# Kernel optimization log

Hardware: AMD Instinct MI355X
Metric: run time of the kernel (lower is better)

## Reference

```python
import jax, jax.numpy as jnp
import numpy as np

N = 2048   # num nodes
D = 512    # hidden_dim


def setup_inputs() -> dict:
    key = jax.random.key(0)
    k1, k2 = jax.random.split(key)
    x = jax.random.normal(k1, (N, D), dtype=jnp.float32)
    # linear: hidden_dim -> 1 (xavier-like scale)
    w = jax.random.normal(k2, (D,), dtype=jnp.float32) * (1.0 / np.sqrt(D))
    b = jnp.zeros((1,), dtype=jnp.float32)
    return {"x": x, "w": w, "b": b}


def reference(x, w, b):
    # euclidean_distance_matrix + linear fused:
    # s[i,j] = sum_d w_d * (x[i,d]-x[j,d])^2 + b
    #        = q_i + q_j - 2*(x*w) @ x^T + b,  q_i = sum_d w_d x[i,d]^2
    xw = x * w                              # [N, D]
    q = jnp.sum(xw * x, axis=1)             # [N]
    cross = xw @ x.T                        # [N, N]
    s = q[:, None] + q[None, :] - 2.0 * cross + b[0]
    grouping_matrix = jax.nn.sigmoid(s)     # [N, N]

    # compute_fielder, similarity_graph='base'
    W = grouping_matrix
    degree = jnp.sum(W, axis=1)
    L = jnp.diag(degree) - W                # symmetric graph Laplacian
    eigen_values, eigen_vectors = jnp.linalg.eigh(L)
    order = jnp.argsort(jnp.abs(eigen_values))
    fielder_value = eigen_values[order[1]]
    fielder_vector = eigen_vectors[:, order[1]]
    return grouping_matrix, fielder_value, fielder_vector
```

## Files before the change

kernel.cpp:

```cpp
#include <hip/hip_runtime.h>
#include <math.h>

constexpr int NN = 2048;
constexpr int DD_ = 512;
constexpr int LM = 64;
constexpr int VS = NN + 32;
constexpr int GPART = 8;
#define SIGN_FLIP 1

__device__ inline double waveReduceSum(double v) {
#pragma unroll
  for (int off = 32; off; off >>= 1) v += __shfl_down(v, off, 64);
  return v;
}

__device__ inline double blockReduceSum256(double v) {
  __shared__ double sm[4];
  int lane = threadIdx.x & 63;
  int wid  = threadIdx.x >> 6;
  v = waveReduceSum(v);
  __syncthreads();
  if (lane == 0) sm[wid] = v;
  __syncthreads();
  double r = 0.0;
  if (threadIdx.x < 4) r = sm[threadIdx.x];
  if (wid == 0) {
    r += __shfl_down(r, 2, 64);
    r += __shfl_down(r, 1, 64);
  }
  return r;
}

__global__ __launch_bounds__(256) void k_q(const float* __restrict__ x,
                                           const float* __restrict__ w,
                                           float* __restrict__ q) {
  int row = blockIdx.x;
  int t = threadIdx.x;
  const float* xr = x + (size_t)row * DD_;
  float acc = 0.f;
#pragma unroll
  for (int p = 0; p < 2; ++p) {
    int d = t + 256 * p;
    float xv = xr[d];
    acc += w[d] * xv * xv;
  }
  double r = blockReduceSum256((double)acc);
  if (t == 0) q[row] = (float)r;
}

__global__ __launch_bounds__(256) void k_W(const float* __restrict__ x,
                                           const float* __restrict__ wv,
                                           const float* __restrict__ q,
                                           const float* __restrict__ bptr,
                                           float* __restrict__ out) {
  __shared__ float As[16][68];
  __shared__ float Bs[16][68];
  const int t = threadIdx.x;
  const int i0 = blockIdx.y * 64, j0 = blockIdx.x * 64;
  const int lr = t >> 4, lk = t & 15;
  const int tr = t >> 4, tc = t & 15;
  float acc[4][4];
#pragma unroll
  for (int a = 0; a < 4; ++a)
#pragma unroll
    for (int b = 0; b < 4; ++b) acc[a][b] = 0.f;

  for (int kk = 0; kk < DD_; kk += 16) {
    float wk = wv[kk + lk];
#pragma unroll
    for (int p = 0; p < 4; ++p) {
      As[lk][lr + 16 * p] = x[(size_t)(i0 + lr + 16 * p) * DD_ + kk + lk] * wk;
      Bs[lk][lr + 16 * p] = x[(size_t)(j0 + lr + 16 * p) * DD_ + kk + lk];
    }
    __syncthreads();
#pragma unroll
    for (int k = 0; k < 16; ++k) {
      float4 av = *(const float4*)&As[k][tr * 4];
      float4 bv = *(const float4*)&Bs[k][tc * 4];
      float aa[4] = {av.x, av.y, av.z, av.w};
      float bb[4] = {bv.x, bv.y, bv.z, bv.w};
#pragma unroll
      for (int a = 0; a < 4; ++a)
#pragma unroll
        for (int b = 0; b < 4; ++b) acc[a][b] += aa[a] * bb[b];
    }
    __syncthreads();
  }
  float b0 = bptr[0];
#pragma unroll
  for (int a = 0; a < 4; ++a) {
    int i = i0 + tr * 4 + a;
    float qi = q[i];
    float4 st;
    float* stp = &st.x;
#pragma unroll
    for (int b = 0; b < 4; ++b) {
      int j = j0 + tc * 4 + b;
      float s = qi + q[j] - 2.0f * acc[a][b] + b0;
      stp[b] = 1.0f / (1.0f + expf(-s));
    }
    *(float4*)&out[(size_t)i * NN + j0 + tc * 4] = st;
  }
}

__global__ __launch_bounds__(256) void k_init(double* __restrict__ r,
                                              double* __restrict__ part) {
  int t = threadIdx.x;
  double loc[8];
  double s = 0.0;
#pragma unroll
  for (int p = 0; p < 8; ++p) {
    unsigned i = (unsigned)(t + 256 * p);
    unsigned u = i * 2654435761u + 0x9E3779B9u;
    u ^= u >> 16; u *= 0x85EBCA6Bu; u ^= u >> 13; u *= 0xC2B2AE35u; u ^= u >> 16;
    double val = ((double)u / 4294967296.0) - 0.5;
    loc[p] = val; s += val;
  }
  __shared__ double mean_s, inv_s;
  double tot = blockReduceSum256(s);
  if (t == 0) mean_s = tot / (double)NN;
  __syncthreads();
  double mean = mean_s;
  double ss = 0.0;
#pragma unroll
  for (int p = 0; p < 8; ++p) { loc[p] -= mean; ss += loc[p] * loc[p]; }
  double tss = blockReduceSum256(ss);
  if (t == 0) inv_s = 1.0 / sqrt(tss);
  __syncthreads();
  double inv = inv_s;
#pragma unroll
  for (int p = 0; p < 8; ++p) r[t + 256 * p] = loc[p] * inv;
  if (t < GPART) part[t] = (t == 0) ? 1.0 : 0.0;
}

__global__ __launch_bounds__(256) void k_mva(const float* __restrict__ Wm,
                                             double* __restrict__ deg,
                                             const double* __restrict__ rprev,
                                             const double* __restrict__ part,
                                             double* __restrict__ V,
                                             double* __restrict__ wstash,
                                             double* __restrict__ c,
                                             double* __restrict__ beta, int j) {
  int b = blockIdx.x, t = threadIdx.x;
  double ss = 0.0;
#pragma unroll
  for (int p = 0; p < GPART; ++p) ss += part[p];
  double bet = sqrt(ss);
  double inv = (bet > 1e-3) ? 1.0 / bet : 0.0;

  if (b < NN) {
    const float* wr = Wm + (size_t)b * NN;
    double acc = 0.0, dsum = 0.0;
    if (j == 0) {
#pragma unroll
      for (int p = 0; p < 2; ++p) {
        int i = 4 * t + 1024 * p;
        float4 wl = *(const float4*)&wr[i];
        dsum += (double)wl.x + (double)wl.y + (double)wl.z + (double)wl.w;
        acc += (double)wl.x * rprev[i] + (double)wl.y * rprev[i + 1] +
               (double)wl.z * rprev[i + 2] + (double)wl.w * rprev[i + 3];
      }
    } else {
#pragma unroll
      for (int p = 0; p < 2; ++p) {
        int i = 4 * t + 1024 * p;
        float4 wl = *(const float4*)&wr[i];
        acc += (double)wl.x * rprev[i] + (double)wl.y * rprev[i + 1] +
               (double)wl.z * rprev[i + 2] + (double)wl.w * rprev[i + 3];
      }
    }
    double red = blockReduceSum256(acc);
    double dred = 0.0;
    if (j == 0) dred = blockReduceSum256(dsum);
    if (t == 0) {
      double d;
      if (j == 0) { d = dred; deg[b] = d; }
      else d = deg[b];
      double vj = rprev[b] * inv;
      V[(size_t)j * VS + b] = vj;
      wstash[(size_t)j * VS + b] = d * vj - red * inv;
      if (b == 0 && j > 0) beta[j - 1] = (bet > 1e-3) ? bet : 0.0;
    }
  } else {
    int q = b - NN;
    const double* wq = wstash + (size_t)q * VS;
    double a = 0.0;
#pragma unroll
    for (int p = 0; p < 8; ++p) { int i = t + 256 * p; a += wq[i] * rprev[i]; }
    double red = blockReduceSum256(a);
    if (t == 0) c[q] = red * inv;
  }
}

__global__ __launch_bounds__(256) void k_orthb(const double* __restrict__ V,
                                               const double* __restrict__ wstash,
                                               const double* __restrict__ c,
                                               double* __restrict__ r,
                                               double* __restrict__ part,
                                               double* __restrict__ alpha, int j) {
  __shared__ double cs[LM];
  __shared__ double cj_s, s1_s;
  int b = blockIdx.x, t = threadIdx.x;
  const double* wj = wstash + (size_t)j * VS;
  const double* vj = V + (size_t)j * VS;
  double a = 0.0, s = 0.0;
#pragma unroll
  for (int p = 0; p < 8; ++p) {
    int i = t + 256 * p;
    double wv = wj[i];
    a += vj[i] * wv;
    s += wv;
  }
  double cj = blockReduceSum256(a);
  double s1 = blockReduceSum256(s);
  if (t == 0) { cj_s = cj; s1_s = s1; }
  for (int k = t; k < j; k += 256) cs[k] = c[k];
  __syncthreads();
  double cjv = cj_s, s1v = s1_s;
  int i = b * 256 + t;
  double val = wj[i] - s1v / (double)NN - cjv * vj[i];
  for (int k = 0; k < j; ++k) val -= cs[k] * V[(size_t)k * VS + i];
  r[i] = val;
  double rr = blockReduceSum256(val * val);
  if (t == 0) {
    part[b] = rr;
    if (b == 0) alpha[j] = cjv;
  }
}

__device__ inline double guardpiv(double d) {
  if (fabs(d) < 1e-280) return (d < 0.0) ? -1e-280 : 1e-280;
  return d;
}

__global__ __launch_bounds__(64) void k_tri(const double* __restrict__ alpha,
                                            const double* __restrict__ beta,
                                            double* __restrict__ svec) {
  __shared__ double al[LM], be[LM];
  __shared__ double Dg[LM], Dl[LM], Du[LM], Du2[LM], bb[LM];
  __shared__ unsigned char piv[LM];
  __shared__ double bounds[2];
  __shared__ int cnts[64];
  __shared__ int meff_s;
  int t = threadIdx.x;
  for (int i = t; i < LM; i += 64) { al[i] = alpha[i]; be[i] = (i < LM - 1) ? beta[i] : 0.0; }
  __syncthreads();
  if (t == 0) {
    int m = LM;
    for (int i = 0; i < LM; ++i) {
      if (!isfinite(al[i])) { m = i; break; }
      if (i < LM - 1 && (be[i] == 0.0 || !isfinite(be[i]))) { m = i + 1; break; }
    }
    if (m < 2) m = 2;
    meff_s = m;
  }
  __syncthreads();
  const int n = meff_s;
  double lo = 1e300, hi = -1e300;
  for (int i = t; i < n; i += 64) {
    double r = 0.0;
    if (i > 0) r += fabs(be[i - 1]);
    if (i < n - 1) r += fabs(be[i]);
    lo = fmin(lo, al[i] - r);
    hi = fmax(hi, al[i] + r);
  }
#pragma unroll
  for (int off = 32; off; off >>= 1) {
    lo = fmin(lo, __shfl_down(lo, off, 64));
    hi = fmax(hi, __shfl_down(hi, off, 64));
  }
  if (t == 0) { bounds[0] = lo; bounds[1] = hi; }
  __syncthreads();
  for (int round = 0; round < 3; ++round) {
    double L0 = bounds[0], H0 = bounds[1];
    double p = L0 + (H0 - L0) * ((double)(t + 1) / 65.0);
    int cnt = 0;
    double d = al[0] - p;
    if (d < 0) cnt++;
    for (int i = 1; i < n; ++i) {
      if (fabs(d) < 1e-300) d = (d < 0.0) ? -1e-300 : 1e-300;
      double bi = be[i - 1];
      d = (al[i] - p) - bi * bi / d;
      if (d < 0) cnt++;
    }
    cnts[t] = cnt;
    __syncthreads();
    if (t == 0) {
      double nl = L0, nh = H0;
      for (int l = 0; l < 64; ++l) {
        double pl = L0 + (H0 - L0) * ((double)(l + 1) / 65.0);
        if (cnts[l] == 0) nl = pl;
        else { nh = pl; break; }
      }
      bounds[0] = nl; bounds[1] = nh;
    }
    __syncthreads();
  }
  double sigma = 0.5 * (bounds[0] + bounds[1]);
  if (t == 0) {
    for (int i = 0; i < n; ++i) Dg[i] = al[i] - sigma;
    for (int i = 0; i < n - 1; ++i) { Dl[i] = be[i]; Du[i] = be[i]; }
    for (int i = 0; i < n - 2; ++i) Du2[i] = 0.0;
    for (int i = 0; i < n - 1; ++i) {
      if (fabs(Dg[i]) >= fabs(Dl[i])) {
        double dpiv = guardpiv(Dg[i]);
        double fact = Dl[i] / dpiv;
        Dl[i] = fact;
        Dg[i + 1] -= fact * Du[i];
        piv[i] = 0;
      } else {
        double fact = Dg[i] / Dl[i];
        Dg[i] = Dl[i]; Dl[i] = fact;
        double temp = Du[i];
        Du[i] = Dg[i + 1];
        Dg[i + 1] = temp - fact * Dg[i + 1];
        if (i < n - 2) { Du2[i] = Du[i + 1]; Du[i + 1] = -fact * Du[i + 1]; }
        piv[i] = 1;
      }
    }
    for (int i = 0; i < n; ++i) bb[i] = 1.0;
    for (int i = 0; i < n - 1; ++i) {
      if (!piv[i]) bb[i + 1] -= Dl[i] * bb[i];
      else { double tmp = bb[i]; bb[i] = bb[i + 1]; bb[i + 1] = tmp - Dl[i] * bb[i]; }
    }
    bb[n - 1] = bb[n - 1] / guardpiv(Dg[n - 1]);
    bb[n - 2] = (bb[n - 2] - Du[n - 2] * bb[n - 1]) / guardpiv(Dg[n - 2]);
    for (int i = n - 3; i >= 0; --i)
      bb[i] = (bb[i] - Du[i] * bb[i + 1] - Du2[i] * bb[i + 2]) / guardpiv(Dg[i]);
    double nrm = 0.0;
    for (int i = 0; i < n; ++i) nrm += bb[i] * bb[i];
    double s = 1.0 / sqrt(nrm);
    for (int i = 0; i < LM; ++i) svec[i] = (i < n) ? bb[i] * s : 0.0;
  }
}

__global__ __launch_bounds__(256) void k_ritz(const double* __restrict__ V,
                                              const double* __restrict__ s,
                                              double* __restrict__ u) {
  __shared__ double cs[LM];
  int t = threadIdx.x;
  for (int k = t; k < LM; k += 256) cs[k] = s[k];
  __syncthreads();
  int i = blockIdx.x * 256 + t;
  double acc = 0.0;
  for (int k = 0; k < LM; ++k) acc += cs[k] * V[(size_t)k * VS + i];
  u[i] = acc;
}

__global__ __launch_bounds__(256) void k_mvu(const float* __restrict__ Wm,
                                             const double* __restrict__ deg,
                                             const double* __restrict__ v,
                                             double* __restrict__ w) {
  int row = blockIdx.x, t = threadIdx.x;
  const float* wr = Wm + (size_t)row * NN;
  double acc = 0.0;
#pragma unroll
  for (int p = 0; p < 2; ++p) {
    int i = 4 * t + 1024 * p;
    float4 wl = *(const float4*)&wr[i];
    acc += (double)wl.x * v[i] + (double)wl.y * v[i + 1] +
           (double)wl.z * v[i + 2] + (double)wl.w * v[i + 3];
  }
  double r = blockReduceSum256(acc);
  if (t == 0) w[row] = deg[row] * v[row] - r;
}

__global__ __launch_bounds__(256) void k_tail(const double* __restrict__ u,
                                              const double* __restrict__ lu,
                                              float* __restrict__ out_lam,
                                              float* __restrict__ outv) {
  __shared__ double mv[256];
  __shared__ int mi[256];
  __shared__ double mean_s, scale_s;
  int t = threadIdx.x;
  double a = 0.0, b = 0.0;
#pragma unroll
  for (int p = 0; p < 8; ++p) {
    int i = t + 256 * p;
    a += u[i] * lu[i];
    b += u[i] * u[i];
  }
  double ra = blockReduceSum256(a);
  double rb = blockReduceSum256(b);
  if (t == 0) *out_lam = (float)(ra / rb);
  double loc[8];
  double s = 0.0;
#pragma unroll
  for (int p = 0; p < 8; ++p) { loc[p] = u[t + 256 * p]; s += loc[p]; }
  double tot = blockReduceSum256(s);
  if (t == 0) mean_s = tot / (double)NN;
  __syncthreads();
  double mean = mean_s;
  double ss = 0.0, bv = -1.0;
  int bi = 0;
#pragma unroll
  for (int p = 0; p < 8; ++p) {
    loc[p] -= mean;
    ss += loc[p] * loc[p];
    double aa = fabs(loc[p]);
    if (aa > bv) { bv = aa; bi = p; }
  }
  double tss = blockReduceSum256(ss);
  mv[t] = bv; mi[t] = t + 256 * bi;
  __syncthreads();
  for (int off = 128; off; off >>= 1) {
    if (t < off) {
      if (mv[t + off] > mv[t]) { mv[t] = mv[t + off]; mi[t] = mi[t + off]; }
    }
    __syncthreads();
  }
  if (t == 0) {
    int gi = mi[0];
    double best = u[gi] - mean_s;
    double sgn = (best < 0.0) ? -1.0 : 1.0;
#if SIGN_FLIP
    sgn = -sgn;
#endif
    scale_s = sgn / sqrt(tss);
  }
  __syncthreads();
  double sc = scale_s;
#pragma unroll
  for (int p = 0; p < 8; ++p) outv[t + 256 * p] = (float)(loc[p] * sc);
}

extern "C" void kernel_launch(void* const* d_in, const int* in_sizes, int n_in,
                              void* d_out, int out_size, void* d_ws, size_t ws_size,
                              hipStream_t stream) {
  const float* x = (const float*)d_in[0];
  const float* wv = (const float*)d_in[1];
  const float* bp = (const float*)d_in[2];
  float* out = (float*)d_out;

  char* ws = (char*)d_ws;
  size_t off = 0;
  auto alloc = [&](size_t bytes) -> char* {
    char* p = ws + off;
    off = (off + bytes + 255) & ~(size_t)255;
    return p;
  };
  float* q      = (float*)alloc((size_t)NN * 4);
  double* deg   = (double*)alloc((size_t)NN * 8);
  double* r     = (double*)alloc((size_t)NN * 8);
  double* u     = (double*)alloc((size_t)NN * 8);
  double* c     = (double*)alloc((size_t)(LM + 2) * 8);
  double* alpha = (double*)alloc((size_t)LM * 8);
  double* beta  = (double*)alloc((size_t)LM * 8);
  double* svec  = (double*)alloc((size_t)LM * 8);
  double* part  = (double*)alloc((size_t)GPART * 8);
  double* V     = (double*)alloc((size_t)LM * VS * 8);
  double* wstash= (double*)alloc((size_t)LM * VS * 8);
  (void)ws_size; (void)in_sizes; (void)n_in; (void)out_size;

  k_q<<<NN, 256, 0, stream>>>(x, wv, q);
  dim3 g(NN / 64, NN / 64);
  k_W<<<g, 256, 0, stream>>>(x, wv, q, bp, out);
  k_init<<<1, 256, 0, stream>>>(r, part);

  for (int j = 0; j < LM; ++j) {
    k_mva<<<NN + j, 256, 0, stream>>>(out, deg, r, part, V, wstash, c, beta, j);
    k_orthb<<<NN / 256, 256, 0, stream>>>(V, wstash, c, r, part, alpha, j);
  }
  k_tri<<<1, 64, 0, stream>>>(alpha, beta, svec);
  k_ritz<<<NN / 256, 256, 0, stream>>>(V, svec, u);
  k_mvu<<<NN, 256, 0, stream>>>(out, deg, u, r);
  k_tail<<<1, 256, 0, stream>>>(u, r, out + (size_t)NN * NN,
                                out + (size_t)NN * NN + 1);
}
```

Before: 842.7 us.

## Compute similarity GEMM with split-bf16 MFMA and double-buffered LDS tiles

Replaces the fp32 CUDA-core tiled GEMM with a 128x128-tile MFMA bf16 kernel using a three-pass hi/lo split (ah*bh + ah*bl + al*bh) to keep near-fp32 accuracy. A new preprocessing kernel computes q and writes hi/lo bf16 copies of x*w and x. The bf16 buffers alias the Lanczos V/wstash workspace, which is only used later. This adds an extra conversion pass and some precision loss from the dropped lo*lo term.

```diff
diff --git a/kernel.cpp b/kernel.cpp
--- a/kernel.cpp
+++ b/kernel.cpp
@@ -8,6 +8,10 @@
 constexpr int GPART = 8;
 #define SIGN_FLIP 1
 
+
+typedef __attribute__((ext_vector_type(4))) float f32x4;
+typedef __attribute__((ext_vector_type(8))) short bf16x8;
+
 __device__ inline double waveReduceSum(double v) {
 #pragma unroll
   for (int off = 32; off; off >>= 1) v += __shfl_down(v, off, 64);
@@ -31,75 +35,147 @@
   return r;
 }
 
-__global__ __launch_bounds__(256) void k_q(const float* __restrict__ x,
-                                           const float* __restrict__ w,
-                                           float* __restrict__ q) {
-  int row = blockIdx.x;
-  int t = threadIdx.x;
-  const float* xr = x + (size_t)row * DD_;
-  float acc = 0.f;
-#pragma unroll
-  for (int p = 0; p < 2; ++p) {
-    int d = t + 256 * p;
-    float xv = xr[d];
-    acc += w[d] * xv * xv;
-  }
-  double r = blockReduceSum256((double)acc);
-  if (t == 0) q[row] = (float)r;
-}
-
-__global__ __launch_bounds__(256) void k_W(const float* __restrict__ x,
-                                           const float* __restrict__ wv,
-                                           const float* __restrict__ q,
-                                           const float* __restrict__ bptr,
-                                           float* __restrict__ out) {
-  __shared__ float As[16][68];
-  __shared__ float Bs[16][68];
+__device__ inline double blockReduceSum128(double v) {
+  __shared__ double sm[2];
+  int lane = threadIdx.x & 63;
+  int wid  = threadIdx.x >> 6;
+  v = waveReduceSum(v);
+  if (lane == 0) sm[wid] = v;
+  __syncthreads();
+  double r = 0.0;
+  if (threadIdx.x == 0) r = sm[0] + sm[1];
+  return r;
+}
+
+__device__ inline unsigned short f2bf(float f) {
+  unsigned u = __float_as_uint(f);
+  u += 0x7FFFu + ((u >> 16) & 1u);
+  return (unsigned short)(u >> 16);
+}
+__device__ inline float bf2f(unsigned short h) {
+  return __uint_as_float(((unsigned)h) << 16);
+}
+
+__global__ __launch_bounds__(128) void k_cvtq(const float* __restrict__ x,
+                                              const float* __restrict__ w,
+                                              float* __restrict__ q,
+                                              unsigned short* __restrict__ ah,
+                                              unsigned short* __restrict__ al,
+                                              unsigned short* __restrict__ bh,
+                                              unsigned short* __restrict__ bl) {
+  int row = blockIdx.x, t = threadIdx.x;
+  int d = 4 * t;
+  float4 xv = *(const float4*)&x[(size_t)row * DD_ + d];
+  float4 wv = *(const float4*)&w[d];
+  float xs[4] = {xv.x, xv.y, xv.z, xv.w};
+  float wsv[4] = {wv.x, wv.y, wv.z, wv.w};
+  unsigned short rah[4], ral[4], rbh[4], rbl[4];
+  float accq = 0.f;
+#pragma unroll
+  for (int kq = 0; kq < 4; ++kq) {
+    float xf = xs[kq], wf = wsv[kq];
+    float a = xf * wf;
+    unsigned short h = f2bf(a);
+    rah[kq] = h;
+    ral[kq] = f2bf(a - bf2f(h));
+    unsigned short hb = f2bf(xf);
+    rbh[kq] = hb;
+    rbl[kq] = f2bf(xf - bf2f(hb));
+    accq += wf * xf * xf;
+  }
+  ushort4 vA = {rah[0], rah[1], rah[2], rah[3]};
+  ushort4 vAl = {ral[0], ral[1], ral[2], ral[3]};
+  ushort4 vB = {rbh[0], rbh[1], rbh[2], rbh[3]};
+  ushort4 vBl = {rbl[0], rbl[1], rbl[2], rbl[3]};
+  *(ushort4*)&ah[(size_t)row * DD_ + d] = vA;
+  *(ushort4*)&al[(size_t)row * DD_ + d] = vAl;
+  *(ushort4*)&bh[(size_t)row * DD_ + d] = vB;
+  *(ushort4*)&bl[(size_t)row * DD_ + d] = vBl;
+  double rq = blockReduceSum128((double)accq);
+  if (t == 0) q[row] = (float)rq;
+}
+
+__global__ __launch_bounds__(256) void k_Wm(const unsigned short* __restrict__ ah,
+                                            const unsigned short* __restrict__ al,
+                                            const unsigned short* __restrict__ bh,
+                                            const unsigned short* __restrict__ bl,
+                                            const float* __restrict__ q,
+                                            const float* __restrict__ bptr,
+                                            float* __restrict__ out) {
+  __shared__ unsigned short As[2][128][40];
+  __shared__ unsigned short Bs[2][128][40];
   const int t = threadIdx.x;
-  const int i0 = blockIdx.y * 64, j0 = blockIdx.x * 64;
-  const int lr = t >> 4, lk = t & 15;
-  const int tr = t >> 4, tc = t & 15;
-  float acc[4][4];
+  const int i0 = blockIdx.y * 128, j0 = blockIdx.x * 128;
+  const int lane = t & 63, wv = t >> 6;
+  const int wr = wv >> 1, wc = wv & 1;
+  const int fr = lane & 15, kc = lane >> 4;
+  const int srow = t >> 1, scol = (t & 1) * 16;
+
+  f32x4 acc[4][4];
 #pragma unroll
   for (int a = 0; a < 4; ++a)
 #pragma unroll
-    for (int b = 0; b < 4; ++b) acc[a][b] = 0.f;
-
-  for (int kk = 0; kk < DD_; kk += 16) {
-    float wk = wv[kk + lk];
-#pragma unroll
-    for (int p = 0; p < 4; ++p) {
-      As[lk][lr + 16 * p] = x[(size_t)(i0 + lr + 16 * p) * DD_ + kk + lk] * wk;
-      Bs[lk][lr + 16 * p] = x[(size_t)(j0 + lr + 16 * p) * DD_ + kk + lk];
+    for (int b = 0; b < 4; ++b) acc[a][b] = (f32x4){0.f, 0.f, 0.f, 0.f};
+
+  {
+    bf16x8 ra0 = *(const bf16x8*)&ah[(size_t)(i0 + srow) * DD_ + scol];
+    bf16x8 ra1 = *(const bf16x8*)&ah[(size_t)(i0 + srow) * DD_ + scol + 8];
+    bf16x8 rb0 = *(const bf16x8*)&bh[(size_t)(j0 + srow) * DD_ + scol];
+    bf16x8 rb1 = *(const bf16x8*)&bh[(size_t)(j0 + srow) * DD_ + scol + 8];
+    *(bf16x8*)&As[0][srow][scol] = ra0;
+    *(bf16x8*)&As[0][srow][scol + 8] = ra1;
+    *(bf16x8*)&Bs[0][srow][scol] = rb0;
+    *(bf16x8*)&Bs[0][srow][scol + 8] = rb1;
+  }
+  __syncthreads();
+  int cur = 0;
+  for (int s = 0; s < 48; ++s) {
+    bf16x8 na0, na1, nb0, nb1;
+    if (s + 1 < 48) {
+      int pass = (s + 1) >> 4;
+      int kk = ((s + 1) & 15) * 32;
+      const unsigned short* srcA = (pass == 2) ? al : ah;
+      const unsigned short* srcB = (pass == 1) ? bl : bh;
+      na0 = *(const bf16x8*)&srcA[(size_t)(i0 + srow) * DD_ + kk + scol];
+      na1 = *(const bf16x8*)&srcA[(size_t)(i0 + srow) * DD_ + kk + scol + 8];
+      nb0 = *(const bf16x8*)&srcB[(size_t)(j0 + srow) * DD_ + kk + scol];
+      nb1 = *(const bf16x8*)&srcB[(size_t)(j0 + srow) * DD_ + kk + scol + 8];
+    }
+    bf16x8 af[4], bq[4];
+#pragma unroll
+    for (int a = 0; a < 4; ++a)
+      af[a] = *(const bf16x8*)&As[cur][wr * 64 + a * 16 + fr][kc * 8];
+#pragma unroll
+    for (int b = 0; b < 4; ++b)
+      bq[b] = *(const bf16x8*)&Bs[cur][wc * 64 + b * 16 + fr][kc * 8];
+#pragma unroll
+    for (int a = 0; a < 4; ++a)
+#pragma unroll
+      for (int b = 0; b < 4; ++b)
+        acc[a][b] = __builtin_amdgcn_mfma_f32_16x16x32_bf16(af[a], bq[b], acc[a][b], 0, 0, 0);
+    if (s + 1 < 48) {
+      *(bf16x8*)&As[cur ^ 1][srow][scol] = na0;
+      *(bf16x8*)&As[cur ^ 1][srow][scol + 8] = na1;
+      *(bf16x8*)&Bs[cur ^ 1][srow][scol] = nb0;
+      *(bf16x8*)&Bs[cur ^ 1][srow][scol + 8] = nb1;
     }
     __syncthreads();
-#pragma unroll
-    for (int k = 0; k < 16; ++k) {
-      float4 av = *(const float4*)&As[k][tr * 4];
-      float4 bv = *(const float4*)&Bs[k][tc * 4];
-      float aa[4] = {av.x, av.y, av.z, av.w};
-      float bb[4] = {bv.x, bv.y, bv.z, bv.w};
-#pragma unroll
-      for (int a = 0; a < 4; ++a)
-#pragma unroll
-        for (int b = 0; b < 4; ++b) acc[a][b] += aa[a] * bb[b];
-    }
-    __syncthreads();
+    cur ^= 1;
   }
   float b0 = bptr[0];
 #pragma unroll
   for (int a = 0; a < 4; ++a) {
-    int i = i0 + tr * 4 + a;
-    float qi = q[i];
-    float4 st;
-    float* stp = &st.x;
-#pragma unroll
-    for (int b = 0; b < 4; ++b) {
-      int j = j0 + tc * 4 + b;
-      float s = qi + q[j] - 2.0f * acc[a][b] + b0;
-      stp[b] = 1.0f / (1.0f + expf(-s));
-    }
-    *(float4*)&out[(size_t)i * NN + j0 + tc * 4] = st;
+#pragma unroll
+    for (int rg = 0; rg < 4; ++rg) {
+      int i = i0 + wr * 64 + a * 16 + kc * 4 + rg;
+      float qi = q[i];
+#pragma unroll
+      for (int b = 0; b < 4; ++b) {
+        int j = j0 + wc * 64 + b * 16 + fr;
+        float s = qi + q[j] - 2.0f * acc[a][b][rg] + b0;
+        out[(size_t)i * NN + j] = 1.0f / (1.0f + expf(-s));
+      }
+    }
   }
 }
 
@@ -448,13 +524,18 @@
   double* beta  = (double*)alloc((size_t)LM * 8);
   double* svec  = (double*)alloc((size_t)LM * 8);
   double* part  = (double*)alloc((size_t)GPART * 8);
-  double* V     = (double*)alloc((size_t)LM * VS * 8);
-  double* wstash= (double*)alloc((size_t)LM * VS * 8);
+  char* un = alloc((size_t)4 * NN * DD_ * 2);
+  unsigned short* ah = (unsigned short*)un;
+  unsigned short* al = ah + (size_t)NN * DD_;
+  unsigned short* bh = al + (size_t)NN * DD_;
+  unsigned short* bl = bh + (size_t)NN * DD_;
+  double* V      = (double*)un;
+  double* wstash = V + (size_t)LM * VS;
   (void)ws_size; (void)in_sizes; (void)n_in; (void)out_size;
 
-  k_q<<<NN, 256, 0, stream>>>(x, wv, q);
-  dim3 g(NN / 64, NN / 64);
-  k_W<<<g, 256, 0, stream>>>(x, wv, q, bp, out);
+  k_cvtq<<<NN, 128, 0, stream>>>(x, wv, q, ah, al, bh, bl);
+  dim3 g(NN / 128, NN / 128);
+  k_Wm<<<g, 256, 0, stream>>>(ah, al, bh, bl, q, bp, out);
   k_init<<<1, 256, 0, stream>>>(r, part);
 
   for (int j = 0; j < LM; ++j) {
```

Result: faster. 820.5 us (-2.6%).
